# Kernel tuning notes

Measured on AMD Instinct MI355X. Metric: run time of the kernel, lower is better.

Reference implementation:

```python
import jax, jax.numpy as jnp
import numpy as np

EPS = 1e-7  # K.epsilon()

def squash(v, axis=-1):
    s2 = jnp.sum(jnp.square(v), axis=axis, keepdims=True)
    scale = s2 / (1.0 + s2) / jnp.sqrt(s2 + EPS)
    return scale * v

def setup_inputs() -> dict:
    key = jax.random.key(0)
    k1, k2 = jax.random.split(key)
    B, I, J, K, M = 32, 64, 1152, 32, 16
    inputs = jax.random.normal(k1, (B, J, M), dtype=jnp.float32)
    # glorot_uniform-scaled init for W [num_capsule, input_num_capsule, dim_capsule, input_dim_capsule]
    limit = np.sqrt(6.0 / (M + K))
    W = jax.random.uniform(k2, (I, J, K, M), dtype=jnp.float32, minval=-limit, maxval=limit)
    return {"inputs": inputs, "W": W}

def reference(inputs, W):
    routings = 3
    # u_hat: [B, I, J, K]
    u_hat = jnp.einsum('ijkm,bjm->bijk', W, inputs)
    B, I, J, _ = u_hat.shape
    b = jnp.zeros((B, I, J), dtype=u_hat.dtype)
    outputs = None
    for i in range(routings):
        c = jax.nn.softmax(b, axis=1)                    # softmax over output capsules
        s = jnp.einsum('bij,bijk->bik', c, u_hat)        # weighted sum over input capsules
        outputs = squash(s)
        if i < routings - 1:
            agreement = jnp.einsum('bik,bijk->bij', outputs, u_hat)
            b = b + agreement
    return outputs
```

## Files before the change

### kernel.cpp

```cpp
#include <hip/hip_runtime.h>


#define Ii 64
#define Jj 1152
#define Kk 32
#define Bb 32
#define NJB2 72

typedef short  bf16x8 __attribute__((ext_vector_type(8)));
typedef float  f32x16 __attribute__((ext_vector_type(16)));
typedef float  f32x4  __attribute__((ext_vector_type(4)));

__device__ __forceinline__ void split2(float a, float b, unsigned &hi, unsigned &lo){
  unsigned ua = __float_as_uint(a), ub = __float_as_uint(b);
  unsigned ha = ua & 0xFFFF0000u, hb = ub & 0xFFFF0000u;
  hi = (ha >> 16) | hb;
  float la = a - __uint_as_float(ha);
  float lb = b - __uint_as_float(hb);
  lo = ((__float_as_uint(la) & 0xFFFF0000u) >> 16) | (__float_as_uint(lb) & 0xFFFF0000u);
}

__device__ __forceinline__ void split8(const float* v, bf16x8 &hi, bf16x8 &lo){
  union U { bf16x8 v; unsigned u[4]; } H, L;
#pragma unroll
  for (int p=0;p<4;p++) split2(v[2*p], v[2*p+1], H.u[p], L.u[p]);
  hi = H.v; lo = L.v;
}

#define MFMA(A,B,C) __builtin_amdgcn_mfma_f32_32x32x16_bf16(A,B,C,0,0,0)

template<int FIRST>
__global__ __launch_bounds__(256, 2)
void k_s(const float* __restrict__ Wp, const ushort* __restrict__ Wbi,
         ushort* __restrict__ Wbo, const float* __restrict__ xp,
         const float* __restrict__ brt, const float* __restrict__ mp,
         const float* __restrict__ zp, float* __restrict__ spart)
{
  __shared__ float red[4*1088];
  const int t  = threadIdx.x;
  const int w  = t >> 6, lane = t & 63;
  const int kk = lane & 31;
  const int h  = lane >> 5;
  const int b  = lane & 31;
  const int i0 = blockIdx.y * 4;
  const int j0 = blockIdx.x * 16 + w * 4;

  bf16x8 Bh[4], Bl[4];
  float mzm[4], mzz[4];
#pragma unroll
  for (int jj=0;jj<4;jj++){
    const int j = j0 + jj;
    float x8[8];
    *(f32x4*)(x8)   = *(const f32x4*)(xp + (b*Jj + j)*16 + h*8);
    *(f32x4*)(x8+4) = *(const f32x4*)(xp + (b*Jj + j)*16 + h*8 + 4);
    split8(x8, Bh[jj], Bl[jj]);
    if (!FIRST){ mzm[jj] = mp[j*32+b]; mzz[jj] = zp[j*32+b]; }
  }

  f32x16 acc[4];
#pragma unroll
  for (int ii=0;ii<4;ii++) acc[ii] = {};

#pragma unroll
  for (int ii=0; ii<4; ++ii){
    const int i = i0 + ii;
#pragma unroll
    for (int jj=0;jj<4;jj++){
      const size_t eoff = (size_t)(i*Jj + j0+jj)*512 + kk*16 + h*8;
      f32x16 d = {};
      if (FIRST){
        float w8[8];
        *(f32x4*)(w8)   = *(const f32x4*)(Wp + eoff);
        *(f32x4*)(w8+4) = *(const f32x4*)(Wp + eoff + 4);
        bf16x8 Ah, Al;
        split8(w8, Ah, Al);
        *reinterpret_cast<bf16x8*>(Wbo + eoff) = Ah;
        d = MFMA(Ah, Bh[jj], d);
        d = MFMA(Ah, Bl[jj], d);
        d = MFMA(Al, Bh[jj], d);
      } else {
        const bf16x8 Ah = *reinterpret_cast<const bf16x8*>(Wbi + eoff);
        d = MFMA(Ah, Bh[jj], d);
        d = MFMA(Ah, Bl[jj], d);
      }
      float cw;
      if (FIRST) cw = 0.015625f;
      else {
        const float bv = brt[(i*Jj + j0+jj)*32 + b];
        cw = __expf(bv - mzm[jj]) * mzz[jj];
      }
#pragma unroll
      for (int r=0;r<16;r++) acc[ii][r] += cw * d[r];
    }
  }

#pragma unroll
  for (int ii=0; ii<4; ++ii){
    __syncthreads();
#pragma unroll
    for (int r=0;r<16;r++) red[w*1088 + lane*17 + r] = acc[ii][r];
    __syncthreads();
    f32x4 outv;
#pragma unroll
    for (int q=0;q<4;q++){
      const int v  = t*4 + q;
      const int lv = v >> 4, r = v & 15;
      float sum = 0.f;
#pragma unroll
      for (int ww=0;ww<4;ww++) sum += red[ww*1088 + lv*17 + r];
      outv[q] = sum;
    }
    *(f32x4*)&spart[((size_t)blockIdx.x*Ii + (i0+ii))*1024 + t*4] = outv;
  }
}

template<int TR>
__global__ __launch_bounds__(256)
void k_redsq(const float* __restrict__ spart, float* __restrict__ outp)
{
  const int i = blockIdx.x, t = threadIdx.x;
  f32x4 a = {0.f,0.f,0.f,0.f};
#pragma unroll 8
  for (int jb=0;jb<NJB2;jb++)
    a += *(const f32x4*)&spart[((size_t)jb*Ii + i)*1024 + t*4];

  const int b2 = (t>>2)&31, hh = t>>7, t3 = t&3;
  float ss = a.x*a.x + a.y*a.y + a.z*a.z + a.w*a.w;
  ss += __shfl_xor(ss,1);
  ss += __shfl_xor(ss,2);
  __shared__ float sp2[2][32];
  if (t3 == 0) sp2[hh][b2] = ss;
  __syncthreads();
  const float s2 = sp2[0][b2] + sp2[1][b2];
  const float scale = s2/(1.f+s2) * rsqrtf(s2 + 1e-7f);
#pragma unroll
  for (int q=0;q<4;q++){
    const int kcap = q + 8*t3 + 4*hh;
    const float val = a[q]*scale;
    if (TR) outp[(i*Kk + kcap)*Bb + b2] = val;
    else    outp[((size_t)b2*Ii + i)*Kk + kcap] = val;
  }
}

template<int ADD>
__global__ __launch_bounds__(256, 2)
void k_ag(const ushort* __restrict__ Wb, const float* __restrict__ xp,
          const float* __restrict__ ot, float* __restrict__ brt)
{
  const int t  = threadIdx.x;
  const int w  = t >> 6, lane = t & 63;
  const int kk = lane & 31;
  const int h  = lane >> 5;
  const int b  = lane & 31;
  const int i0 = blockIdx.y * 4;
  const int j0 = blockIdx.x * 16 + w * 4;

  bf16x8 Bh[4], Bl[4];
#pragma unroll
  for (int jj=0;jj<4;jj++){
    const int j = j0 + jj;
    float x8[8];
    *(f32x4*)(x8)   = *(const f32x4*)(xp + (b*Jj + j)*16 + h*8);
    *(f32x4*)(x8+4) = *(const f32x4*)(xp + (b*Jj + j)*16 + h*8 + 4);
    split8(x8, Bh[jj], Bl[jj]);
  }

#pragma unroll
  for (int ii=0; ii<4; ++ii){
    const int i = i0 + ii;
    float ov[16];
#pragma unroll
    for (int r=0;r<16;r++){
      const int kcap = (r & 3) + 8*(r >> 2) + 4*h;
      ov[r] = ot[(i*Kk + kcap)*Bb + b];
    }
#pragma unroll
    for (int jj=0;jj<4;jj++){
      const size_t eoff = (size_t)(i*Jj + j0+jj)*512 + kk*16 + h*8;
      const bf16x8 Ah = *reinterpret_cast<const bf16x8*>(Wb + eoff);
      f32x16 d = {};
      d = MFMA(Ah, Bh[jj], d);
      d = MFMA(Ah, Bl[jj], d);
      float ap = 0.f;
#pragma unroll
      for (int r=0;r<16;r++) ap += ov[r]*d[r];
      ap += __shfl_xor(ap, 32);
      if (h == 0){
        const int idx = (i*Jj + j0+jj)*32 + b;
        const float prev = ADD ? brt[idx] : 0.f;
        brt[idx] = prev + ap;
      }
    }
  }
}

__global__ __launch_bounds__(256)
void k_norm(const float* __restrict__ brt, float* __restrict__ mp,
            float* __restrict__ zp)
{
  const int t  = threadIdx.x;
  const int jl = t >> 5, b = t & 31;
  const int j  = blockIdx.x*8 + jl;
  float v[64];
  float mx = -1e30f;
#pragma unroll
  for (int ii=0; ii<64; ++ii){
    v[ii] = brt[(ii*Jj + j)*32 + b];
    mx = fmaxf(mx, v[ii]);
  }
  float sum = 0.f;
#pragma unroll
  for (int ii=0; ii<64; ++ii) sum += __expf(v[ii]-mx);
  mp[j*32 + b] = mx;
  zp[j*32 + b] = 1.f/sum;
}

extern "C" void kernel_launch(void* const* d_in, const int* in_sizes, int n_in,
                              void* d_out, int out_size, void* d_ws, size_t ws_size,
                              hipStream_t stream)
{
  const float* x  = (const float*)d_in[0];
  const float* Wp = (const float*)d_in[1];
  float* out = (float*)d_out;
  float* ws  = (float*)d_ws;
  float* spart = ws;
  float* br    = ws + 4718592;
  float* m     = ws + 7077888;
  float* z     = ws + 7114752;
  float* ot    = ws + 7151616;
  ushort* Wbf  = (ushort*)(ws + 7217152);

  dim3 gs(NJB2, 16), bs(256);

  k_s<1><<<gs, bs, 0, stream>>>(Wp, nullptr, Wbf, x, nullptr, nullptr, nullptr, spart);
  k_redsq<1><<<dim3(64), bs, 0, stream>>>(spart, ot);
  k_ag<0><<<gs, bs, 0, stream>>>(Wbf, x, ot, br);
  k_norm<<<dim3(144), bs, 0, stream>>>(br, m, z);

  k_s<0><<<gs, bs, 0, stream>>>(nullptr, Wbf, nullptr, x, br, m, z, spart);
  k_redsq<1><<<dim3(64), bs, 0, stream>>>(spart, ot);
  k_ag<1><<<gs, bs, 0, stream>>>(Wbf, x, ot, br);
  k_norm<<<dim3(144), bs, 0, stream>>>(br, m, z);

  k_s<0><<<gs, bs, 0, stream>>>(nullptr, Wbf, nullptr, x, br, m, z, spart);
  k_redsq<0><<<dim3(64), bs, 0, stream>>>(spart, out);
}
```

Measured before the change: 142.3 us.

## Fuse softmax normalizer into agreement kernel and store partial sums as bf16

Removes the separate k_norm kernel. The agreement kernel now accumulates exp(b) per (j,b) and atomically adds it into a zeroed denominator buffer, so the softmax is computed without subtracting the max. The partial sums from k_s are also rounded to bf16, which halves the write and read traffic of the reduction. In exchange this risks exp overflow when logits grow, adds bf16 rounding error to s, and adds memsets and atomics.

Result: faster. 136.3 us (-4.2%).

```diff
diff --git a/kernel.cpp b/kernel.cpp
--- a/kernel.cpp
+++ b/kernel.cpp
@@ -27,14 +27,19 @@
   hi = H.v; lo = L.v;
 }
 
+__device__ __forceinline__ ushort f2bf_rne(float f){
+  unsigned u = __float_as_uint(f);
+  return (ushort)((u + 0x7FFFu + ((u >> 16) & 1u)) >> 16);
+}
+
 #define MFMA(A,B,C) __builtin_amdgcn_mfma_f32_32x32x16_bf16(A,B,C,0,0,0)
 
 template<int FIRST>
 __global__ __launch_bounds__(256, 2)
 void k_s(const float* __restrict__ Wp, const ushort* __restrict__ Wbi,
          ushort* __restrict__ Wbo, const float* __restrict__ xp,
-         const float* __restrict__ brt, const float* __restrict__ mp,
-         const float* __restrict__ zp, float* __restrict__ spart)
+         const float* __restrict__ brt, const float* __restrict__ zp,
+         ushort* __restrict__ spart)
 {
   __shared__ float red[4*1088];
   const int t  = threadIdx.x;
@@ -46,7 +51,7 @@
   const int j0 = blockIdx.x * 16 + w * 4;
 
   bf16x8 Bh[4], Bl[4];
-  float mzm[4], mzz[4];
+  float zi[4];
 #pragma unroll
   for (int jj=0;jj<4;jj++){
     const int j = j0 + jj;
@@ -54,7 +59,7 @@
     *(f32x4*)(x8)   = *(const f32x4*)(xp + (b*Jj + j)*16 + h*8);
     *(f32x4*)(x8+4) = *(const f32x4*)(xp + (b*Jj + j)*16 + h*8 + 4);
     split8(x8, Bh[jj], Bl[jj]);
-    if (!FIRST){ mzm[jj] = mp[j*32+b]; mzz[jj] = zp[j*32+b]; }
+    if (!FIRST) zi[jj] = 1.0f / zp[j*32 + b];
   }
 
   f32x16 acc[4];
@@ -87,7 +92,7 @@
       if (FIRST) cw = 0.015625f;
       else {
         const float bv = brt[(i*Jj + j0+jj)*32 + b];
-        cw = __expf(bv - mzm[jj]) * mzz[jj];
+        cw = __expf(bv) * zi[jj];
       }
 #pragma unroll
       for (int r=0;r<16;r++) acc[ii][r] += cw * d[r];
@@ -100,32 +105,42 @@
 #pragma unroll
     for (int r=0;r<16;r++) red[w*1088 + lane*17 + r] = acc[ii][r];
     __syncthreads();
-    f32x4 outv;
-#pragma unroll
-    for (int q=0;q<4;q++){
-      const int v  = t*4 + q;
-      const int lv = v >> 4, r = v & 15;
-      float sum = 0.f;
-#pragma unroll
-      for (int ww=0;ww<4;ww++) sum += red[ww*1088 + lv*17 + r];
-      outv[q] = sum;
-    }
-    *(f32x4*)&spart[((size_t)blockIdx.x*Ii + (i0+ii))*1024 + t*4] = outv;
+    ushort4 outv;
+    {
+      float sx, sy, sz, sw;
+#pragma unroll
+      for (int q=0;q<4;q++){
+        const int v  = t*4 + q;
+        const int lv = v >> 4, r = v & 15;
+        float sum = 0.f;
+#pragma unroll
+        for (int ww=0;ww<4;ww++) sum += red[ww*1088 + lv*17 + r];
+        if (q==0) sx=sum; else if (q==1) sy=sum; else if (q==2) sz=sum; else sw=sum;
+      }
+      outv.x = f2bf_rne(sx); outv.y = f2bf_rne(sy);
+      outv.z = f2bf_rne(sz); outv.w = f2bf_rne(sw);
+    }
+    *(ushort4*)&spart[((size_t)blockIdx.x*Ii + (i0+ii))*1024 + t*4] = outv;
   }
 }
 
 template<int TR>
 __global__ __launch_bounds__(256)
-void k_redsq(const float* __restrict__ spart, float* __restrict__ outp)
+void k_redsq(const ushort* __restrict__ spart, float* __restrict__ outp)
 {
   const int i = blockIdx.x, t = threadIdx.x;
-  f32x4 a = {0.f,0.f,0.f,0.f};
+  float a0=0.f, a1=0.f, a2=0.f, a3=0.f;
 #pragma unroll 8
-  for (int jb=0;jb<NJB2;jb++)
-    a += *(const f32x4*)&spart[((size_t)jb*Ii + i)*1024 + t*4];
+  for (int jb=0;jb<NJB2;jb++){
+    const ushort4 u = *(const ushort4*)&spart[((size_t)jb*Ii + i)*1024 + t*4];
+    a0 += __uint_as_float((unsigned)u.x << 16);
+    a1 += __uint_as_float((unsigned)u.y << 16);
+    a2 += __uint_as_float((unsigned)u.z << 16);
+    a3 += __uint_as_float((unsigned)u.w << 16);
+  }
 
   const int b2 = (t>>2)&31, hh = t>>7, t3 = t&3;
-  float ss = a.x*a.x + a.y*a.y + a.z*a.z + a.w*a.w;
+  float ss = a0*a0 + a1*a1 + a2*a2 + a3*a3;
   ss += __shfl_xor(ss,1);
   ss += __shfl_xor(ss,2);
   __shared__ float sp2[2][32];
@@ -133,19 +148,20 @@
   __syncthreads();
   const float s2 = sp2[0][b2] + sp2[1][b2];
   const float scale = s2/(1.f+s2) * rsqrtf(s2 + 1e-7f);
+  const float vals[4] = {a0*scale, a1*scale, a2*scale, a3*scale};
 #pragma unroll
   for (int q=0;q<4;q++){
     const int kcap = q + 8*t3 + 4*hh;
-    const float val = a[q]*scale;
-    if (TR) outp[(i*Kk + kcap)*Bb + b2] = val;
-    else    outp[((size_t)b2*Ii + i)*Kk + kcap] = val;
+    if (TR) outp[(i*Kk + kcap)*Bb + b2] = vals[q];
+    else    outp[((size_t)b2*Ii + i)*Kk + kcap] = vals[q];
   }
 }
 
 template<int ADD>
 __global__ __launch_bounds__(256, 2)
 void k_ag(const ushort* __restrict__ Wb, const float* __restrict__ xp,
-          const float* __restrict__ ot, float* __restrict__ brt)
+          const float* __restrict__ ot, float* __restrict__ brt,
+          float* __restrict__ zp)
 {
   const int t  = threadIdx.x;
   const int w  = t >> 6, lane = t & 63;
@@ -165,6 +181,8 @@
     split8(x8, Bh[jj], Bl[jj]);
   }
 
+  float ez[4] = {0.f, 0.f, 0.f, 0.f};
+
 #pragma unroll
   for (int ii=0; ii<4; ++ii){
     const int i = i0 + ii;
@@ -188,31 +206,17 @@
       if (h == 0){
         const int idx = (i*Jj + j0+jj)*32 + b;
         const float prev = ADD ? brt[idx] : 0.f;
-        brt[idx] = prev + ap;
-      }
-    }
-  }
-}
-
-__global__ __launch_bounds__(256)
-void k_norm(const float* __restrict__ brt, float* __restrict__ mp,
-            float* __restrict__ zp)
-{
-  const int t  = threadIdx.x;
-  const int jl = t >> 5, b = t & 31;
-  const int j  = blockIdx.x*8 + jl;
-  float v[64];
-  float mx = -1e30f;
-#pragma unroll
-  for (int ii=0; ii<64; ++ii){
-    v[ii] = brt[(ii*Jj + j)*32 + b];
-    mx = fmaxf(mx, v[ii]);
-  }
-  float sum = 0.f;
-#pragma unroll
-  for (int ii=0; ii<64; ++ii) sum += __expf(v[ii]-mx);
-  mp[j*32 + b] = mx;
-  zp[j*32 + b] = 1.f/sum;
+        const float bn = prev + ap;
+        brt[idx] = bn;
+        ez[jj] += __expf(bn);
+      }
+    }
+  }
+  if (h == 0){
+#pragma unroll
+    for (int jj=0;jj<4;jj++)
+      atomicAdd(&zp[(j0+jj)*32 + b], ez[jj]);
+  }
 }
 
 extern "C" void kernel_launch(void* const* d_in, const int* in_sizes, int n_in,
@@ -223,25 +227,24 @@
   const float* Wp = (const float*)d_in[1];
   float* out = (float*)d_out;
   float* ws  = (float*)d_ws;
-  float* spart = ws;
-  float* br    = ws + 4718592;
-  float* m     = ws + 7077888;
-  float* z     = ws + 7114752;
-  float* ot    = ws + 7151616;
-  ushort* Wbf  = (ushort*)(ws + 7217152);
+  ushort* spart = (ushort*)ws;
+  float* br    = ws + 2359296;
+  float* z     = ws + 4718592;
+  float* ot    = ws + 4755456;
+  ushort* Wbf  = (ushort*)(ws + 4820992);
 
   dim3 gs(NJB2, 16), bs(256);
 
-  k_s<1><<<gs, bs, 0, stream>>>(Wp, nullptr, Wbf, x, nullptr, nullptr, nullptr, spart);
+  k_s<1><<<gs, bs, 0, stream>>>(Wp, nullptr, Wbf, x, nullptr, nullptr, spart);
   k_redsq<1><<<dim3(64), bs, 0, stream>>>(spart, ot);
-  k_ag<0><<<gs, bs, 0, stream>>>(Wbf, x, ot, br);
-  k_norm<<<dim3(144), bs, 0, stream>>>(br, m, z);
-
-  k_s<0><<<gs, bs, 0, stream>>>(nullptr, Wbf, nullptr, x, br, m, z, spart);
+  hipMemsetAsync(z, 0, 36864*sizeof(float), stream);
+  k_ag<0><<<gs, bs, 0, stream>>>(Wbf, x, ot, br, z);
+
+  k_s<0><<<gs, bs, 0, stream>>>(nullptr, Wbf, nullptr, x, br, z, spart);
   k_redsq<1><<<dim3(64), bs, 0, stream>>>(spart, ot);
-  k_ag<1><<<gs, bs, 0, stream>>>(Wbf, x, ot, br);
-  k_norm<<<dim3(144), bs, 0, stream>>>(br, m, z);
-
-  k_s<0><<<gs, bs, 0, stream>>>(nullptr, Wbf, nullptr, x, br, m, z, spart);
+  hipMemsetAsync(z, 0, 36864*sizeof(float), stream);
+  k_ag<1><<<gs, bs, 0, stream>>>(Wbf, x, ot, br, z);
+
+  k_s<0><<<gs, bs, 0, stream>>>(nullptr, Wbf, nullptr, x, br, z, spart);
   k_redsq<0><<<dim3(64), bs, 0, stream>>>(spart, out);
 }
```
